# Kernel optimization log

Hardware: AMD Instinct MI355X
Metric: run time of the kernel (lower is better)

The kernel has to match this reference:

```python
import jax, jax.numpy as jnp
import numpy as np

B, T, D = 4, 4096, 1024


def setup_inputs() -> dict:
    key = jax.random.key(0)
    ks = jax.random.split(key, 10)
    scale = 1.0 / np.sqrt(D)
    x = jax.random.normal(ks[0], (B, T, D), jnp.float32)
    last_x = jnp.zeros((D,), jnp.float32)
    last_num = jnp.zeros((D,), jnp.float32)
    last_den = jnp.zeros((D,), jnp.float32)
    time_decay = jax.random.normal(ks[1], (D,), jnp.float32) * 0.1
    time_first = jax.random.normal(ks[2], (D,), jnp.float32) * 0.1
    time_mix_k = jax.random.uniform(ks[3], (1, 1, D), jnp.float32)
    time_mix_v = jax.random.uniform(ks[4], (1, 1, D), jnp.float32)
    time_mix_r = jax.random.uniform(ks[5], (1, 1, D), jnp.float32)
    Wk = jax.random.normal(ks[6], (D, D), jnp.float32) * scale
    Wv = jax.random.normal(ks[7], (D, D), jnp.float32) * scale
    Wr = jax.random.normal(ks[8], (D, D), jnp.float32) * scale
    Wo = jax.random.normal(ks[9], (D, D), jnp.float32) * scale
    return {"x": x, "last_x": last_x, "last_num": last_num, "last_den": last_den,
            "time_decay": time_decay, "time_first": time_first,
            "time_mix_k": time_mix_k, "time_mix_v": time_mix_v, "time_mix_r": time_mix_r,
            "Wk": Wk, "Wv": Wv, "Wr": Wr, "Wo": Wo}


def reference(x, last_x, last_num, last_den, time_decay, time_first,
              time_mix_k, time_mix_v, time_mix_r, Wk, Wv, Wr, Wo):
    # token-shift lerps against the incoming state (broadcast over B, T)
    k = jnp.einsum('btd,ed->bte', x * time_mix_k + last_x * (1.0 - time_mix_k), Wk)
    v = jnp.einsum('btd,ed->bte', x * time_mix_v + last_x * (1.0 - time_mix_v), Wv)
    r = jnp.einsum('btd,ed->bte', x * time_mix_r + last_x * (1.0 - time_mix_r), Wr)
    # WKV numerics, exactly as the original (no extra stabilization)
    efk = jnp.exp(time_first + k)          # exp(time_first + k), [B,T,D]
    wkv = (last_num + efk * v) / (last_den + efk)
    rwkv = jax.nn.sigmoid(r) * wkv
    decay = jnp.exp(-jnp.exp(time_decay))  # [D]
    ek = jnp.exp(k)
    num = decay * last_num + ek * v
    den = decay * last_den + ek
    out = jnp.einsum('btd,ed->bte', rwkv, Wo)
    return out, x[..., -1, :], num[..., -1, :], den[..., -1, :]
```

## Files before the change

### kernel.cpp

```cpp
#include <hip/hip_runtime.h>
#include <cstdint>
#include <cstddef>

constexpr int DD = 1024;
constexpr int TT = 4096;
constexpr int BB = 4;
constexpr int MM = BB * TT;

typedef __bf16 bf16x8 __attribute__((ext_vector_type(8)));
typedef float  f32x4  __attribute__((ext_vector_type(4)));

__device__ __forceinline__ unsigned short f2bf(float f) {
  union { float f; uint32_t u; } c; c.f = f;
  uint32_t r = (c.u + 0x7FFFu + ((c.u >> 16) & 1u)) >> 16;
  return (unsigned short)r;
}

__device__ __forceinline__ void async_ld16(const unsigned short* g, unsigned short* lds_dst) {
  __builtin_amdgcn_global_load_lds(
      (const __attribute__((address_space(1))) void*)g,
      (__attribute__((address_space(3))) void*)lds_dst,
      16, 0, 0);
}

__global__ void prep_wb(const float* __restrict__ Wk, const float* __restrict__ Wv,
                        const float* __restrict__ Wr, const float* __restrict__ Wo,
                        const float* __restrict__ tmk, const float* __restrict__ tmv,
                        const float* __restrict__ tmr,
                        const float* __restrict__ last_x,
                        unsigned short* __restrict__ wz,
                        unsigned short* __restrict__ wo,
                        float* __restrict__ bias) {
  int w = (blockIdx.x * 256 + threadIdx.x) >> 6;
  int lane = threadIdx.x & 63;
  int z = w >> 10;
  int e = w & (DD - 1);
  const float* W  = (z == 0) ? Wk  : (z == 1) ? Wv  : (z == 2) ? Wr : Wo;
  const float* tm = (z == 0) ? tmk : (z == 1) ? tmv : tmr;
  unsigned short* dst = (z < 3) ? (wz + (size_t)z * DD * DD + (size_t)e * DD)
                                : (wo + (size_t)e * DD);
  float s = 0.f;
#pragma unroll
  for (int j = 0; j < 4; ++j) {
    int d = j * 256 + lane * 4;
    float4 wv4 = *(const float4*)(W + (size_t)e * DD + d);
    if (z < 3) {
      float4 t4 = *(const float4*)(tm + d);
      float4 l4 = *(const float4*)(last_x + d);
      s += l4.x * (1.f - t4.x) * wv4.x + l4.y * (1.f - t4.y) * wv4.y +
           l4.z * (1.f - t4.z) * wv4.z + l4.w * (1.f - t4.w) * wv4.w;
      wv4.x *= t4.x; wv4.y *= t4.y; wv4.z *= t4.z; wv4.w *= t4.w;
    }
    ushort4 o;
    o.x = f2bf(wv4.x); o.y = f2bf(wv4.y); o.z = f2bf(wv4.z); o.w = f2bf(wv4.w);
    *(ushort4*)(dst + d) = o;
  }
  if (z < 3) {
    for (int off = 32; off; off >>= 1) s += __shfl_down(s, off, 64);
    if (lane == 0) bias[z * DD + e] = s;
  }
}

__global__ void cvt_x(const float4* __restrict__ x, ushort4* __restrict__ xb,
                      float4* __restrict__ out_xlast) {
  int i = blockIdx.x * 256 + threadIdx.x;
  float4 v = x[i];
  ushort4 o;
  o.x = f2bf(v.x); o.y = f2bf(v.y); o.z = f2bf(v.z); o.w = f2bf(v.w);
  xb[i] = o;
  int m = i >> 8;
  if ((m & (TT - 1)) == (TT - 1)) {
    int b = m >> 12;
    out_xlast[b * 256 + (i & 255)] = v;
  }
}

__global__ __launch_bounds__(256, 2) void gemm_kvr(
    const unsigned short* __restrict__ A,
    const unsigned short* __restrict__ Wz,
    const float* __restrict__ bias,
    const float* __restrict__ time_first, const float* __restrict__ time_decay,
    const float* __restrict__ last_num, const float* __restrict__ last_den,
    unsigned short* __restrict__ rwkv,
    float* __restrict__ out_num, float* __restrict__ out_den) {
  __shared__ unsigned short lA[128 * 32];
  __shared__ unsigned short lB[3][64 * 32];
  const int tid  = threadIdx.x;
  const int lane = tid & 63;
  const int wave = tid >> 6;
  const int n0 = blockIdx.x * 64;
  const int m0 = blockIdx.y * 128;
  const int wm = (wave >> 1) * 64;
  const int wn = (wave & 1) * 32;

  f32x4 acc[3][4][2] = {};

  const int fr_row = lane & 15;
  const int fr_kb  = (lane >> 4) * 16;
  const int srow = tid >> 2;
  const int scol = (tid & 3) * 8;

  for (int k0 = 0; k0 < DD; k0 += 32) {
    __syncthreads();
#pragma unroll
    for (int it = 0; it < 2; ++it) {
      int cc  = it * 256 + tid;
      int row = cc >> 2;
      async_ld16(A + (size_t)(m0 + row) * DD + (k0 + scol),
                 lA + (size_t)(it * 256 + wave * 64) * 8);
    }
#pragma unroll
    for (int z = 0; z < 3; ++z) {
      async_ld16(Wz + (size_t)z * DD * DD + (size_t)(n0 + srow) * DD + (k0 + scol),
                 lB[z] + (size_t)(wave * 64) * 8);
    }
    __syncthreads();

    bf16x8 af[4], bfr[3][2];
#pragma unroll
    for (int i = 0; i < 4; ++i)
      af[i] = *(const bf16x8*)((const char*)lA + ((wm + i * 16 + fr_row) * 64 + fr_kb));
#pragma unroll
    for (int z = 0; z < 3; ++z)
#pragma unroll
      for (int j = 0; j < 2; ++j)
        bfr[z][j] = *(const bf16x8*)((const char*)lB[z] + ((wn + j * 16 + fr_row) * 64 + fr_kb));

#pragma unroll
    for (int mi = 0; mi < 4; ++mi)
#pragma unroll
      for (int z = 0; z < 3; ++z)
#pragma unroll
        for (int ni = 0; ni < 2; ++ni)
          acc[z][mi][ni] = __builtin_amdgcn_mfma_f32_16x16x32_bf16(
              af[mi], bfr[z][ni], acc[z][mi][ni], 0, 0, 0);
  }

  const int crow = (lane >> 4) * 4;
  const int ccol = lane & 15;
#pragma unroll
  for (int ni = 0; ni < 2; ++ni) {
    int gnz = n0 + wn + ni * 16 + ccol;
    float bk = bias[gnz], bv = bias[DD + gnz], br = bias[2 * DD + gnz];
    float tf = time_first[gnz];
    float ln = last_num[gnz], ld = last_den[gnz];
#pragma unroll
    for (int mi = 0; mi < 4; ++mi) {
#pragma unroll
      for (int r = 0; r < 4; ++r) {
        int gm = m0 + wm + mi * 16 + crow + r;
        float kk = acc[0][mi][ni][r] + bk;
        float vv = acc[1][mi][ni][r] + bv;
        float rr = acc[2][mi][ni][r] + br;
        float efk = __expf(tf + kk);
        float wkv = (ln + efk * vv) / (ld + efk);
        float sr  = 1.0f / (1.0f + __expf(-rr));
        rwkv[(size_t)gm * DD + gnz] = f2bf(sr * wkv);
        if ((gm & (TT - 1)) == (TT - 1)) {
          int b = gm >> 12;
          float dec = __expf(-__expf(time_decay[gnz]));
          float ek  = __expf(kk);
          out_num[b * DD + gnz] = dec * ln + ek * vv;
          out_den[b * DD + gnz] = dec * ld + ek;
        }
      }
    }
  }
}

__global__ void gemm_bt128(const unsigned short* __restrict__ A,
                           const unsigned short* __restrict__ Bw,
                           float* __restrict__ Cf,
                           int M, int N, int K) {
  __shared__ unsigned short lA[128 * 32];
  __shared__ unsigned short lB[128 * 32];
  const int tid  = threadIdx.x;
  const int lane = tid & 63;
  const int wave = tid >> 6;
  const int n0 = blockIdx.x * 128;
  const int m0 = blockIdx.y * 128;
  const int wm = (wave >> 1) * 64;
  const int wn = (wave & 1) * 64;

  f32x4 acc[4][4] = {};
  const int fr_row = lane & 15;
  const int fr_kb  = (lane >> 4) * 16;

  for (int k0 = 0; k0 < K; k0 += 32) {
    __syncthreads();
#pragma unroll
    for (int it = 0; it < 2; ++it) {
      int cc  = it * 256 + wave * 64 + lane;
      int row = cc >> 2;
      int col = (cc & 3) * 8;
      async_ld16(A + (size_t)(m0 + row) * K + (k0 + col),
                 lA + (size_t)(it * 256 + wave * 64) * 8);
    }
#pragma unroll
    for (int it = 0; it < 2; ++it) {
      int cc  = it * 256 + wave * 64 + lane;
      int row = cc >> 2;
      int col = (cc & 3) * 8;
      async_ld16(Bw + (size_t)(n0 + row) * K + (k0 + col),
                 lB + (size_t)(it * 256 + wave * 64) * 8);
    }
    __syncthreads();

    bf16x8 af[4], bfr[4];
#pragma unroll
    for (int i = 0; i < 4; ++i) {
      af[i]  = *(const bf16x8*)((const char*)lA + ((wm + i * 16 + fr_row) * 64 + fr_kb));
      bfr[i] = *(const bf16x8*)((const char*)lB + ((wn + i * 16 + fr_row) * 64 + fr_kb));
    }
#pragma unroll
    for (int mi = 0; mi < 4; ++mi)
#pragma unroll
      for (int ni = 0; ni < 4; ++ni)
        acc[mi][ni] = __builtin_amdgcn_mfma_f32_16x16x32_bf16(af[mi], bfr[ni], acc[mi][ni], 0, 0, 0);
  }

  const int crow = (lane >> 4) * 4;
  const int ccol = lane & 15;
#pragma unroll
  for (int mi = 0; mi < 4; ++mi) {
#pragma unroll
    for (int ni = 0; ni < 4; ++ni) {
      int gn = n0 + wn + ni * 16 + ccol;
#pragma unroll
      for (int r = 0; r < 4; ++r) {
        int gm = m0 + wm + mi * 16 + crow + r;
        Cf[(size_t)gm * N + gn] = acc[mi][ni][r];
      }
    }
  }
}

extern "C" void kernel_launch(void* const* d_in, const int* in_sizes, int n_in,
                              void* d_out, int out_size, void* d_ws, size_t ws_size,
                              hipStream_t stream) {
  const float* x          = (const float*)d_in[0];
  const float* last_x     = (const float*)d_in[1];
  const float* last_num   = (const float*)d_in[2];
  const float* last_den   = (const float*)d_in[3];
  const float* time_decay = (const float*)d_in[4];
  const float* time_first = (const float*)d_in[5];
  const float* tmk        = (const float*)d_in[6];
  const float* tmv        = (const float*)d_in[7];
  const float* tmr        = (const float*)d_in[8];
  const float* Wk         = (const float*)d_in[9];
  const float* Wv         = (const float*)d_in[10];
  const float* Wr         = (const float*)d_in[11];
  const float* Wo         = (const float*)d_in[12];

  float* out       = (float*)d_out;
  float* out_xlast = out + (size_t)MM * DD;
  float* out_num   = out_xlast + BB * DD;
  float* out_den   = out_num + BB * DD;

  char* ws = (char*)d_ws;
  unsigned short* xb   = (unsigned short*)ws;
  unsigned short* wz   = (unsigned short*)(ws + 33554432);
  unsigned short* wo   = (unsigned short*)(ws + 39845888);
  float*          bias = (float*)(ws + 41943040);
  unsigned short* rwkv = (unsigned short*)(ws + 41955328);

  prep_wb<<<(4 * DD * 64) / 256, 256, 0, stream>>>(
      Wk, Wv, Wr, Wo, tmk, tmv, tmr, last_x, wz, wo, bias);
  cvt_x<<<(MM * DD / 4) / 256, 256, 0, stream>>>(
      (const float4*)x, (ushort4*)xb, (float4*)out_xlast);

  gemm_kvr<<<dim3(DD / 64, MM / 128), 256, 0, stream>>>(
      xb, wz, bias, time_first, time_decay, last_num, last_den,
      rwkv, out_num, out_den);

  gemm_bt128<<<dim3(DD / 128, MM / 128), 256, 0, stream>>>(
      rwkv, wo, out, MM, DD, DD);
}
```

Measured before the change: 316.8 us.

## Merge prep kernels, double K-step per sync in GEMMs, use fast reciprocal

Merges the weight-prep and x-conversion kernels into one launch. Both GEMMs now load two 32-wide K slices per barrier pair, halving the number of __syncthreads per tile while doubling LDS use. The epilogue divisions are replaced with hardware reciprocal approximations. The larger LDS footprint may lower occupancy, and this is still not a true overlapped double buffer.

```diff
diff --git a/kernel.cpp b/kernel.cpp
--- a/kernel.cpp
+++ b/kernel.cpp
@@ -14,6 +14,10 @@
   union { float f; uint32_t u; } c; c.f = f;
   uint32_t r = (c.u + 0x7FFFu + ((c.u >> 16) & 1u)) >> 16;
   return (unsigned short)r;
+}
+
+__device__ __forceinline__ float fast_rcp(float x) {
+  return __builtin_amdgcn_rcpf(x);
 }
 
 __device__ __forceinline__ void async_ld16(const unsigned short* g, unsigned short* lds_dst) {
@@ -23,55 +27,57 @@
       16, 0, 0);
 }
 
-__global__ void prep_wb(const float* __restrict__ Wk, const float* __restrict__ Wv,
-                        const float* __restrict__ Wr, const float* __restrict__ Wo,
-                        const float* __restrict__ tmk, const float* __restrict__ tmv,
-                        const float* __restrict__ tmr,
-                        const float* __restrict__ last_x,
-                        unsigned short* __restrict__ wz,
-                        unsigned short* __restrict__ wo,
-                        float* __restrict__ bias) {
-  int w = (blockIdx.x * 256 + threadIdx.x) >> 6;
-  int lane = threadIdx.x & 63;
-  int z = w >> 10;
-  int e = w & (DD - 1);
-  const float* W  = (z == 0) ? Wk  : (z == 1) ? Wv  : (z == 2) ? Wr : Wo;
-  const float* tm = (z == 0) ? tmk : (z == 1) ? tmv : tmr;
-  unsigned short* dst = (z < 3) ? (wz + (size_t)z * DD * DD + (size_t)e * DD)
-                                : (wo + (size_t)e * DD);
-  float s = 0.f;
-#pragma unroll
-  for (int j = 0; j < 4; ++j) {
-    int d = j * 256 + lane * 4;
-    float4 wv4 = *(const float4*)(W + (size_t)e * DD + d);
+__global__ void prep_all(const float* __restrict__ Wk, const float* __restrict__ Wv,
+                         const float* __restrict__ Wr, const float* __restrict__ Wo,
+                         const float* __restrict__ tmk, const float* __restrict__ tmv,
+                         const float* __restrict__ tmr,
+                         const float* __restrict__ last_x,
+                         const float4* __restrict__ x,
+                         unsigned short* __restrict__ wz,
+                         unsigned short* __restrict__ wo,
+                         float* __restrict__ bias,
+                         ushort4* __restrict__ xb,
+                         float4* __restrict__ out_xlast) {
+  if (blockIdx.x < 1024) {
+    int w = (blockIdx.x * 256 + threadIdx.x) >> 6;
+    int lane = threadIdx.x & 63;
+    int z = w >> 10;
+    int e = w & (DD - 1);
+    const float* W  = (z == 0) ? Wk  : (z == 1) ? Wv  : (z == 2) ? Wr : Wo;
+    const float* tm = (z == 0) ? tmk : (z == 1) ? tmv : tmr;
+    unsigned short* dst = (z < 3) ? (wz + (size_t)z * DD * DD + (size_t)e * DD)
+                                  : (wo + (size_t)e * DD);
+    float s = 0.f;
+#pragma unroll
+    for (int j = 0; j < 4; ++j) {
+      int d = j * 256 + lane * 4;
+      float4 wv4 = *(const float4*)(W + (size_t)e * DD + d);
+      if (z < 3) {
+        float4 t4 = *(const float4*)(tm + d);
+        float4 l4 = *(const float4*)(last_x + d);
+        s += l4.x * (1.f - t4.x) * wv4.x + l4.y * (1.f - t4.y) * wv4.y +
+             l4.z * (1.f - t4.z) * wv4.z + l4.w * (1.f - t4.w) * wv4.w;
+        wv4.x *= t4.x; wv4.y *= t4.y; wv4.z *= t4.z; wv4.w *= t4.w;
+      }
+      ushort4 o;
+      o.x = f2bf(wv4.x); o.y = f2bf(wv4.y); o.z = f2bf(wv4.z); o.w = f2bf(wv4.w);
+      *(ushort4*)(dst + d) = o;
+    }
     if (z < 3) {
-      float4 t4 = *(const float4*)(tm + d);
-      float4 l4 = *(const float4*)(last_x + d);
-      s += l4.x * (1.f - t4.x) * wv4.x + l4.y * (1.f - t4.y) * wv4.y +
-           l4.z * (1.f - t4.z) * wv4.z + l4.w * (1.f - t4.w) * wv4.w;
-      wv4.x *= t4.x; wv4.y *= t4.y; wv4.z *= t4.z; wv4.w *= t4.w;
-    }
+      for (int off = 32; off; off >>= 1) s += __shfl_down(s, off, 64);
+      if (lane == 0) bias[z * DD + e] = s;
+    }
+  } else {
+    int i = (blockIdx.x - 1024) * 256 + threadIdx.x;
+    float4 v = x[i];
     ushort4 o;
-    o.x = f2bf(wv4.x); o.y = f2bf(wv4.y); o.z = f2bf(wv4.z); o.w = f2bf(wv4.w);
-    *(ushort4*)(dst + d) = o;
-  }
-  if (z < 3) {
-    for (int off = 32; off; off >>= 1) s += __shfl_down(s, off, 64);
-    if (lane == 0) bias[z * DD + e] = s;
-  }
-}
-
-__global__ void cvt_x(const float4* __restrict__ x, ushort4* __restrict__ xb,
-                      float4* __restrict__ out_xlast) {
-  int i = blockIdx.x * 256 + threadIdx.x;
-  float4 v = x[i];
-  ushort4 o;
-  o.x = f2bf(v.x); o.y = f2bf(v.y); o.z = f2bf(v.z); o.w = f2bf(v.w);
-  xb[i] = o;
-  int m = i >> 8;
-  if ((m & (TT - 1)) == (TT - 1)) {
-    int b = m >> 12;
-    out_xlast[b * 256 + (i & 255)] = v;
+    o.x = f2bf(v.x); o.y = f2bf(v.y); o.z = f2bf(v.z); o.w = f2bf(v.w);
+    xb[i] = o;
+    int m = i >> 8;
+    if ((m & (TT - 1)) == (TT - 1)) {
+      int b = m >> 12;
+      out_xlast[b * 256 + (i & 255)] = v;
+    }
   }
 }
 
@@ -83,8 +89,8 @@
     const float* __restrict__ last_num, const float* __restrict__ last_den,
     unsigned short* __restrict__ rwkv,
     float* __restrict__ out_num, float* __restrict__ out_den) {
-  __shared__ unsigned short lA[128 * 32];
-  __shared__ unsigned short lB[3][64 * 32];
+  __shared__ unsigned short lA[2][128 * 32];
+  __shared__ unsigned short lB[2][3][64 * 32];
   const int tid  = threadIdx.x;
   const int lane = tid & 63;
   const int wave = tid >> 6;
@@ -100,40 +106,47 @@
   const int srow = tid >> 2;
   const int scol = (tid & 3) * 8;
 
-  for (int k0 = 0; k0 < DD; k0 += 32) {
-    __syncthreads();
-#pragma unroll
-    for (int it = 0; it < 2; ++it) {
-      int cc  = it * 256 + tid;
-      int row = cc >> 2;
-      async_ld16(A + (size_t)(m0 + row) * DD + (k0 + scol),
-                 lA + (size_t)(it * 256 + wave * 64) * 8);
-    }
-#pragma unroll
-    for (int z = 0; z < 3; ++z) {
-      async_ld16(Wz + (size_t)z * DD * DD + (size_t)(n0 + srow) * DD + (k0 + scol),
-                 lB[z] + (size_t)(wave * 64) * 8);
-    }
-    __syncthreads();
-
-    bf16x8 af[4], bfr[3][2];
-#pragma unroll
-    for (int i = 0; i < 4; ++i)
-      af[i] = *(const bf16x8*)((const char*)lA + ((wm + i * 16 + fr_row) * 64 + fr_kb));
-#pragma unroll
-    for (int z = 0; z < 3; ++z)
-#pragma unroll
-      for (int j = 0; j < 2; ++j)
-        bfr[z][j] = *(const bf16x8*)((const char*)lB[z] + ((wn + j * 16 + fr_row) * 64 + fr_kb));
-
-#pragma unroll
-    for (int mi = 0; mi < 4; ++mi)
+  for (int k0 = 0; k0 < DD; k0 += 64) {
+    __syncthreads();
+#pragma unroll
+    for (int h = 0; h < 2; ++h) {
+      int kk = k0 + h * 32;
+#pragma unroll
+      for (int it = 0; it < 2; ++it) {
+        int cc  = it * 256 + tid;
+        int row = cc >> 2;
+        async_ld16(A + (size_t)(m0 + row) * DD + (kk + scol),
+                   lA[h] + (size_t)(it * 256 + wave * 64) * 8);
+      }
+#pragma unroll
+      for (int z = 0; z < 3; ++z) {
+        async_ld16(Wz + (size_t)z * DD * DD + (size_t)(n0 + srow) * DD + (kk + scol),
+                   lB[h][z] + (size_t)(wave * 64) * 8);
+      }
+    }
+    __syncthreads();
+
+#pragma unroll
+    for (int h = 0; h < 2; ++h) {
+      bf16x8 af[4], bfr[3][2];
+#pragma unroll
+      for (int i = 0; i < 4; ++i)
+        af[i] = *(const bf16x8*)((const char*)lA[h] + ((wm + i * 16 + fr_row) * 64 + fr_kb));
 #pragma unroll
       for (int z = 0; z < 3; ++z)
 #pragma unroll
-        for (int ni = 0; ni < 2; ++ni)
-          acc[z][mi][ni] = __builtin_amdgcn_mfma_f32_16x16x32_bf16(
-              af[mi], bfr[z][ni], acc[z][mi][ni], 0, 0, 0);
+        for (int j = 0; j < 2; ++j)
+          bfr[z][j] = *(const bf16x8*)((const char*)lB[h][z] + ((wn + j * 16 + fr_row) * 64 + fr_kb));
+
+#pragma unroll
+      for (int mi = 0; mi < 4; ++mi)
+#pragma unroll
+        for (int z = 0; z < 3; ++z)
+#pragma unroll
+          for (int ni = 0; ni < 2; ++ni)
+            acc[z][mi][ni] = __builtin_amdgcn_mfma_f32_16x16x32_bf16(
+                af[mi], bfr[z][ni], acc[z][mi][ni], 0, 0, 0);
+    }
   }
 
   const int crow = (lane >> 4) * 4;
@@ -153,8 +166,8 @@
         float vv = acc[1][mi][ni][r] + bv;
         float rr = acc[2][mi][ni][r] + br;
         float efk = __expf(tf + kk);
-        float wkv = (ln + efk * vv) / (ld + efk);
-        float sr  = 1.0f / (1.0f + __expf(-rr));
+        float wkv = (ln + efk * vv) * fast_rcp(ld + efk);
+        float sr  = fast_rcp(1.0f + __expf(-rr));
         rwkv[(size_t)gm * DD + gnz] = f2bf(sr * wkv);
         if ((gm & (TT - 1)) == (TT - 1)) {
           int b = gm >> 12;
@@ -172,8 +185,8 @@
                            const unsigned short* __restrict__ Bw,
                            float* __restrict__ Cf,
                            int M, int N, int K) {
-  __shared__ unsigned short lA[128 * 32];
-  __shared__ unsigned short lB[128 * 32];
+  __shared__ unsigned short lA[2][128 * 32];
+  __shared__ unsigned short lB[2][128 * 32];
   const int tid  = threadIdx.x;
   const int lane = tid & 63;
   const int wave = tid >> 6;
@@ -185,38 +198,44 @@
   f32x4 acc[4][4] = {};
   const int fr_row = lane & 15;
   const int fr_kb  = (lane >> 4) * 16;
-
-  for (int k0 = 0; k0 < K; k0 += 32) {
-    __syncthreads();
-#pragma unroll
-    for (int it = 0; it < 2; ++it) {
-      int cc  = it * 256 + wave * 64 + lane;
-      int row = cc >> 2;
-      int col = (cc & 3) * 8;
-      async_ld16(A + (size_t)(m0 + row) * K + (k0 + col),
-                 lA + (size_t)(it * 256 + wave * 64) * 8);
-    }
-#pragma unroll
-    for (int it = 0; it < 2; ++it) {
-      int cc  = it * 256 + wave * 64 + lane;
-      int row = cc >> 2;
-      int col = (cc & 3) * 8;
-      async_ld16(Bw + (size_t)(n0 + row) * K + (k0 + col),
-                 lB + (size_t)(it * 256 + wave * 64) * 8);
-    }
-    __syncthreads();
-
-    bf16x8 af[4], bfr[4];
-#pragma unroll
-    for (int i = 0; i < 4; ++i) {
-      af[i]  = *(const bf16x8*)((const char*)lA + ((wm + i * 16 + fr_row) * 64 + fr_kb));
-      bfr[i] = *(const bf16x8*)((const char*)lB + ((wn + i * 16 + fr_row) * 64 + fr_kb));
-    }
-#pragma unroll
-    for (int mi = 0; mi < 4; ++mi)
-#pragma unroll
-      for (int ni = 0; ni < 4; ++ni)
-        acc[mi][ni] = __builtin_amdgcn_mfma_f32_16x16x32_bf16(af[mi], bfr[ni], acc[mi][ni], 0, 0, 0);
+  const int scol = (tid & 3) * 8;
+
+  for (int k0 = 0; k0 < K; k0 += 64) {
+    __syncthreads();
+#pragma unroll
+    for (int h = 0; h < 2; ++h) {
+      int kk = k0 + h * 32;
+#pragma unroll
+      for (int it = 0; it < 2; ++it) {
+        int cc  = it * 256 + tid;
+        int row = cc >> 2;
+        async_ld16(A + (size_t)(m0 + row) * K + (kk + scol),
+                   lA[h] + (size_t)(it * 256 + wave * 64) * 8);
+      }
+#pragma unroll
+      for (int it = 0; it < 2; ++it) {
+        int cc  = it * 256 + tid;
+        int row = cc >> 2;
+        async_ld16(Bw + (size_t)(n0 + row) * K + (kk + scol),
+                   lB[h] + (size_t)(it * 256 + wave * 64) * 8);
+      }
+    }
+    __syncthreads();
+
+#pragma unroll
+    for (int h = 0; h < 2; ++h) {
+      bf16x8 af[4], bfr[4];
+#pragma unroll
+      for (int i = 0; i < 4; ++i) {
+        af[i]  = *(const bf16x8*)((const char*)lA[h] + ((wm + i * 16 + fr_row) * 64 + fr_kb));
+        bfr[i] = *(const bf16x8*)((const char*)lB[h] + ((wn + i * 16 + fr_row) * 64 + fr_kb));
+      }
+#pragma unroll
+      for (int mi = 0; mi < 4; ++mi)
+#pragma unroll
+        for (int ni = 0; ni < 4; ++ni)
+          acc[mi][ni] = __builtin_amdgcn_mfma_f32_16x16x32_bf16(af[mi], bfr[ni], acc[mi][ni], 0, 0, 0);
+    }
   }
 
   const int crow = (lane >> 4) * 4;
@@ -264,10 +283,9 @@
   float*          bias = (float*)(ws + 41943040);
   unsigned short* rwkv = (unsigned short*)(ws + 41955328);
 
-  prep_wb<<<(4 * DD * 64) / 256, 256, 0, stream>>>(
-      Wk, Wv, Wr, Wo, tmk, tmv, tmr, last_x, wz, wo, bias);
-  cvt_x<<<(MM * DD / 4) / 256, 256, 0, stream>>>(
-      (const float4*)x, (ushort4*)xb, (float4*)out_xlast);
+  prep_all<<<1024 + MM * DD / 4 / 256, 256, 0, stream>>>(
+      Wk, Wv, Wr, Wo, tmk, tmv, tmr, last_x, (const float4*)x,
+      wz, wo, bias, (ushort4*)xb, (float4*)out_xlast);
 
   gemm_kvr<<<dim3(DD / 64, MM / 128), 256, 0, stream>>>(
       xb, wz, bias, time_first, time_decay, last_num, last_den,
```

After: 301.1 us. 5.0% less time.
